# Kernel tuning notes

Hardware: AMD Instinct MI355X
Metric: run time of the kernel (lower is better)

The kernel has to match this reference:

```python
import jax, jax.numpy as jnp
import numpy as np

A, U, ANT, D2, H = 128, 8, 64, 64, 256
NUE = A * U            # 1024 ues
E_INT = A * NUE        # 131072 interferes edges (all ap x ue pairs)
E_DL = NUE             # one d_link edge per ue


def _mlp(x, Wa, ba, Wb, bb):
    return jax.nn.relu(x @ Wa + ba) @ Wb + bb


def setup_inputs() -> dict:
    key = jax.random.key(0)
    ks = jax.random.split(key, 14)
    f32 = jnp.float32
    inp = {
        'pl_int_re': jax.random.normal(ks[0], (E_INT, ANT), f32) * 0.1,
        'pl_int_im': jax.random.normal(ks[1], (E_INT, ANT), f32) * 0.1,
        'pl_dl_re': jax.random.normal(ks[2], (E_DL, ANT), f32) * 0.1,
        'pl_dl_im': jax.random.normal(ks[3], (E_DL, ANT), f32) * 0.1,
        'pv_re': jax.random.normal(ks[4], (A, U, ANT), f32) * 0.1,
        'pv_im': jax.random.normal(ks[5], (A, U, ANT), f32) * 0.1,
        'W2a': jax.random.normal(ks[6], (4 * ANT, H), f32) / np.sqrt(4 * ANT),
        'b2a': jnp.zeros((H,), f32),
        'W2b': jax.random.normal(ks[7], (H, D2), f32) / np.sqrt(H),
        'b2b': jnp.zeros((D2,), f32),
        'W1a': jax.random.normal(ks[8], (1 + 2 * ANT + D2, H), f32) / np.sqrt(1 + 2 * ANT + D2),
        'b1a': jnp.zeros((H,), f32),
        'W1b': jax.random.normal(ks[9], (H, 2 * ANT), f32) / np.sqrt(H),
        'b1b': jnp.zeros((2 * ANT,), f32),
        # interferes: every ap -> every ue
        'int_src': jnp.repeat(jnp.arange(A, dtype=jnp.int32), NUE),
        'int_dst': jnp.tile(jnp.arange(NUE, dtype=jnp.int32), A),
        # d_link: ap a -> ues [a*U, (a+1)*U)
        'dl_src': jnp.repeat(jnp.arange(A, dtype=jnp.int32), U),
        'dl_dst': jnp.arange(NUE, dtype=jnp.int32),
    }
    return inp


def reference(pl_int_re, pl_int_im, pl_dl_re, pl_dl_im, pv_re, pv_im,
              W2a, b2a, W2b, b2b, W1a, b1a, W1b, b1b,
              int_src, int_dst, dl_src, dl_dst):
    pv = jax.lax.complex(pv_re, pv_im)            # [A,U,ANT] ap power_vector
    pl_int = jax.lax.complex(pl_int_re, pl_int_im)  # [E_INT,ANT]
    pl_dl = jax.lax.complex(pl_dl_re, pl_dl_im)     # [E_DL,ANT]

    def aggregate_interferes(pv_cur):
        src_sum = jnp.sum(pv_cur, axis=1)[int_src]              # [E,ANT]
        infer_vec = src_sum.conj() * pl_int                      # [E,ANT]
        sum_ap = jnp.sum(jnp.abs(infer_vec) ** 2, axis=-1)       # ||.||^2 -> [E]
        return jax.ops.segment_sum(sum_ap[:, None], int_dst, num_segments=NUE)  # [NUE,1]

    # 1) aggregate_interferes (stored in graph; recomputed at the end)
    _ = aggregate_interferes(pv)

    # 2) mlp_aggregate_interferes
    src_sum = jnp.sum(pv, axis=1)[int_src]                       # [E,ANT] complex
    feats = jnp.concatenate([pl_int, src_sum], axis=1)           # [E,2*ANT] complex
    cat_feats = jnp.concatenate([feats.real, feats.imag], axis=1)  # [E,4*ANT]
    msg2 = _mlp(cat_feats, W2a, b2a, W2b, b2b)                   # [E,D2]
    mlp_ue_all = jax.ops.segment_sum(msg2, int_dst, num_segments=NUE)  # [NUE,D2]

    # 3) update_ue_power_vector (d_link edges)
    src_pv_dl = pv[dl_src]                                       # [E_DL,U,ANT]
    iner = jnp.einsum('eua,ea->eu', src_pv_dl.conj(), pl_dl)     # bmm -> [E_DL,U]
    norm1 = jnp.abs(iner) ** 2                                   # [E_DL,U]
    mask1 = jnp.ones((E_DL, U), norm1.dtype).at[jnp.arange(E_DL), dl_dst % U].set(0.0)
    in_infer = jnp.sum(norm1 * mask1, axis=1)[:, None]           # [E_DL,1]

    feat1 = jnp.concatenate([in_infer, pl_dl.real, pl_dl.imag, mlp_ue_all[dl_dst]], axis=1)
    out1 = _mlp(feat1, W1a, b1a, W1b, b1b).reshape(E_DL, 2, ANT)  # [E_DL,2,ANT]
    ue_pv_msg = jax.lax.complex(out1[:, 0, :], out1[:, 1, :])    # [E_DL,ANT]
    # each ue receives exactly one message
    ue_pv = jnp.zeros((NUE, ANT), ue_pv_msg.dtype).at[dl_dst].set(ue_pv_msg)

    # 4) update_ap_power_vector (u_link: ue i -> ap i//U; mailbox [A,U,ANT])
    mailbox = ue_pv.reshape(A, U, ANT)
    flat = mailbox.reshape(A, U * ANT)
    row_sums = jnp.sum(jnp.abs(flat), axis=-1, keepdims=True)
    pv_new = (flat / row_sums).reshape(A, U, ANT)

    # 5) final aggregate_interferes with updated power vectors
    ue_all_interference = aggregate_interferes(pv_new)

    out_stacked = jnp.stack([pv_new.real, pv_new.imag])          # [2,A,U,ANT]
    return out_stacked, ue_all_interference
```

## Files before the change

kernel.cpp:

```cpp
#include <hip/hip_runtime.h>
#include <hip/hip_bf16.h>
#include <hip/hip_fp16.h>

#define A_NUM 128
#define U_NUM 8
#define ANT 64
#define D2 64
#define H_DIM 256
#define NUE 1024
#define E_INT 131072

typedef __attribute__((ext_vector_type(8))) short bf16x8_t;
typedef __attribute__((ext_vector_type(4))) float f32x4_t;

static __device__ inline unsigned short f2bf(float x) {
    unsigned int u = __float_as_uint(x);
    unsigned int r = (u + 0x7fffu + ((u >> 16) & 1u)) >> 16;
    return (unsigned short)r;
}
static __device__ inline unsigned int pack2(float a, float b) {
    return (unsigned int)f2bf(a) | ((unsigned int)f2bf(b) << 16);
}
static __device__ inline float bf2f(unsigned short s) {
    return __uint_as_float(((unsigned int)s) << 16);
}

__global__ void prep_kernel(const float* __restrict__ pv_re, const float* __restrict__ pv_im,
                            const float* __restrict__ W2a, const float* __restrict__ b2a,
                            const float* __restrict__ W2b,
                            const float* __restrict__ W1a, const float* __restrict__ W1b,
                            float* __restrict__ Sa, unsigned short* __restrict__ WpT,
                            unsigned short* __restrict__ W2bT,
                            float* __restrict__ W1aT, float* __restrict__ W1bT) {
    int bid = blockIdx.x, t = threadIdx.x;
    if (bid < A_NUM) {
        __shared__ float sre[ANT], sim[ANT];
        if (t < ANT) {
            float s = 0.f;
            for (int u = 0; u < U_NUM; ++u) s += pv_re[bid * 512 + u * 64 + t];
            sre[t] = s;
        } else if (t < 2 * ANT) {
            int ant = t - ANT;
            float s = 0.f;
            for (int u = 0; u < U_NUM; ++u) s += pv_im[bid * 512 + u * 64 + ant];
            sim[ant] = s;
        }
        __syncthreads();
        float acc = b2a[t];
        for (int ant = 0; ant < ANT; ++ant) {
            acc += sre[ant] * W2a[(64 + ant) * H_DIM + t];
            acc += sim[ant] * W2a[(192 + ant) * H_DIM + t];
        }
        Sa[bid * H_DIM + t] = acc;
    } else if (bid < 136) {
        int base = (bid - A_NUM) * 256 + t;
        for (int i = base; i < 32768 + 16384; i += 8 * 256) {
            if (i < 32768) {
                int h = i >> 7, k = i & 127;
                int row = (k < 64) ? k : (k + 64);
                WpT[i] = f2bf(W2a[row * H_DIM + h]);
            } else {
                int i2 = i - 32768;
                int d = i2 >> 8, k2 = i2 & 255;
                W2bT[i2] = f2bf(W2b[k2 * D2 + d]);
            }
        }
    } else {
        for (int i = (bid - 136) * 256 + t; i < 53248 + 32768; i += 32 * 256) {
            if (i < 53248) {
                int h = i / 208, k = i % 208;
                W1aT[i] = (k < 193) ? W1a[k * 256 + h] : 0.f;
            } else {
                int i2 = i - 53248;
                int c = i2 >> 8, k = i2 & 255;
                W1bT[i2] = W1b[k * 128 + c];
            }
        }
    }
}

__global__ __launch_bounds__(256, 3) void mlp2_kernel(
        const float* __restrict__ plre, const float* __restrict__ plim,
        const float* __restrict__ Sa, const unsigned short* __restrict__ WpT,
        const unsigned short* __restrict__ W2bT, float* __restrict__ partial,
        unsigned short* __restrict__ Pws) {
    __shared__ __attribute__((aligned(16))) unsigned short F[32][136];
    __shared__ __attribute__((aligned(16))) unsigned short Hl[32][264];
    int bid = blockIdx.x;
    int jt_idx = bid & 31, ac = bid >> 5;
    int j0 = jt_idx * 32, a0 = ac * 8;
    int t = threadIdx.x, w = t >> 6, l = t & 63, lm = l & 15, lk = l >> 4;

    int er = t >> 3, seg = t & 7;
    const float* stage_base = (seg < 4) ? plre : plim;
    int stage_off = (j0 + er) * 64 + (seg & 3) * 16;
    int col = ((seg < 4) ? 0 : 64) + (seg & 3) * 16;

    f32x4_t acc2[2];
    acc2[0] = (f32x4_t){0.f, 0.f, 0.f, 0.f};
    acc2[1] = (f32x4_t){0.f, 0.f, 0.f, 0.f};

    float4 stg0, stg1, stg2, stg3;
    {
        const float* p = stage_base + a0 * 65536 + stage_off;
        stg0 = *reinterpret_cast<const float4*>(p);
        stg1 = *reinterpret_cast<const float4*>(p + 4);
        stg2 = *reinterpret_cast<const float4*>(p + 8);
        stg3 = *reinterpret_cast<const float4*>(p + 12);
    }

    for (int ai = 0; ai < 8; ++ai) {
        int a = a0 + ai;
        {
            unsigned int pk0 = pack2(stg0.x, stg0.y), pk1 = pack2(stg0.z, stg0.w);
            unsigned int pk2 = pack2(stg1.x, stg1.y), pk3 = pack2(stg1.z, stg1.w);
            unsigned int pk4 = pack2(stg2.x, stg2.y), pk5 = pack2(stg2.z, stg2.w);
            unsigned int pk6 = pack2(stg3.x, stg3.y), pk7 = pack2(stg3.z, stg3.w);
            *reinterpret_cast<uint4*>(&F[er][col]) = make_uint4(pk0, pk1, pk2, pk3);
            *reinterpret_cast<uint4*>(&F[er][col + 8]) = make_uint4(pk4, pk5, pk6, pk7);
        }
        __syncthreads();
        {
            uint4 rr = *reinterpret_cast<const uint4*>(&F[er][seg * 8]);
            uint4 ri = *reinterpret_cast<const uint4*>(&F[er][64 + seg * 8]);
            const unsigned short* pr = (const unsigned short*)&rr;
            const unsigned short* pi = (const unsigned short*)&ri;
            unsigned int pk[4];
#pragma unroll
            for (int i = 0; i < 4; ++i) {
                float re0 = bf2f(pr[2 * i]), im0 = bf2f(pi[2 * i]);
                float re1 = bf2f(pr[2 * i + 1]), im1 = bf2f(pi[2 * i + 1]);
                unsigned short h0 = __half_as_ushort(__float2half(re0 * re0 + im0 * im0));
                unsigned short h1 = __half_as_ushort(__float2half(re1 * re1 + im1 * im1));
                pk[i] = (unsigned int)h0 | ((unsigned int)h1 << 16);
            }
            *reinterpret_cast<uint4*>(&Pws[(unsigned)(a * 1024 + j0 + er) * 64 + seg * 8]) =
                make_uint4(pk[0], pk[1], pk[2], pk[3]);
        }
        if (ai < 7) {
            const float* p = stage_base + (a0 + ai + 1) * 65536 + stage_off;
            stg0 = *reinterpret_cast<const float4*>(p);
            stg1 = *reinterpret_cast<const float4*>(p + 4);
            stg2 = *reinterpret_cast<const float4*>(p + 8);
            stg3 = *reinterpret_cast<const float4*>(p + 12);
        }
        f32x4_t acc1[2][4];
#pragma unroll
        for (int ht = 0; ht < 4; ++ht) {
            float sa = Sa[a * H_DIM + w * 64 + ht * 16 + lm];
            f32x4_t v = (f32x4_t){sa, sa, sa, sa};
            acc1[0][ht] = v;
            acc1[1][ht] = v;
        }
#pragma unroll
        for (int kc = 0; kc < 4; ++kc) {
            bf16x8_t bfr[4];
#pragma unroll
            for (int ht = 0; ht < 4; ++ht) {
                int h = w * 64 + ht * 16 + lm;
                bfr[ht] = *reinterpret_cast<const bf16x8_t*>(WpT + h * 128 + kc * 32 + lk * 8);
            }
#pragma unroll
            for (int jt = 0; jt < 2; ++jt) {
                bf16x8_t afr = *reinterpret_cast<const bf16x8_t*>(&F[jt * 16 + lm][kc * 32 + lk * 8]);
#pragma unroll
                for (int ht = 0; ht < 4; ++ht)
                    acc1[jt][ht] = __builtin_amdgcn_mfma_f32_16x16x32_bf16(afr, bfr[ht], acc1[jt][ht], 0, 0, 0);
            }
        }
#pragma unroll
        for (int jt = 0; jt < 2; ++jt)
#pragma unroll
            for (int ht = 0; ht < 4; ++ht)
#pragma unroll
                for (int r = 0; r < 4; ++r) {
                    int j = jt * 16 + lk * 4 + r;
                    int h = w * 64 + ht * 16 + lm;
                    float v = acc1[jt][ht][r];
                    Hl[j][h] = f2bf(v > 0.f ? v : 0.f);
                }
        __syncthreads();
        int d = w * 16 + lm;
#pragma unroll
        for (int kc = 0; kc < 8; ++kc) {
            bf16x8_t b2 = *reinterpret_cast<const bf16x8_t*>(W2bT + d * 256 + kc * 32 + lk * 8);
#pragma unroll
            for (int jt = 0; jt < 2; ++jt) {
                bf16x8_t a2 = *reinterpret_cast<const bf16x8_t*>(&Hl[jt * 16 + lm][kc * 32 + lk * 8]);
                acc2[jt] = __builtin_amdgcn_mfma_f32_16x16x32_bf16(a2, b2, acc2[jt], 0, 0, 0);
            }
        }
    }
#pragma unroll
    for (int jt = 0; jt < 2; ++jt)
#pragma unroll
        for (int r = 0; r < 4; ++r) {
            int j = j0 + jt * 16 + lk * 4 + r;
            int d = w * 16 + lm;
            partial[ac * 65536 + j * 64 + d] = acc2[jt][r];
        }
}

__global__ __launch_bounds__(512) void dlink_norm(
        const float* __restrict__ pv_re, const float* __restrict__ pv_im,
        const float* __restrict__ pldre, const float* __restrict__ pldim,
        const float* __restrict__ partial, const float* __restrict__ b2b,
        const float* __restrict__ W1aT, const float* __restrict__ b1a,
        const float* __restrict__ W1bT, const float* __restrict__ b1b,
        float* __restrict__ Q, float* __restrict__ out) {
    int a = blockIdx.x, t = threadIdx.x, w = t >> 6, l = t & 63;
    __shared__ float pvr[512], pvi[512], pldr[512], pldi[512];
    __shared__ float nrm[8][8];
    __shared__ __attribute__((aligned(16))) float feat[8][212];
    __shared__ __attribute__((aligned(16))) float h1[8][260];
    __shared__ float red2[2][8][128];
    __shared__ __attribute__((aligned(16))) float o1[8][128];
    __shared__ float redn[8];
    __shared__ float SshInv;

    pvr[t] = pv_re[a * 512 + t];
    pvi[t] = pv_im[a * 512 + t];
    pldr[t] = pldre[a * 512 + t];
    pldi[t] = pldim[a * 512 + t];
    {
        float acc = 128.f * b2b[t & 63];
#pragma unroll
        for (int c = 0; c < 16; ++c) acc += partial[c * 65536 + a * 512 + t];
        feat[t >> 6][129 + (t & 63)] = acc;
    }
    if (t < 152) feat[t / 19][193 + t % 19] = 0.f;
    __syncthreads();
    feat[t >> 6][1 + (t & 63)] = pldr[t];
    feat[t >> 6][65 + (t & 63)] = pldi[t];
#pragma unroll
    for (int p = 0; p < 8; ++p) {
        int idx = w * 8 + p;
        int el = idx >> 3, u = idx & 7;
        float pr = pvr[u * 64 + l], pi = pvi[u * 64 + l];
        float qr = pldr[el * 64 + l], qi = pldi[el * 64 + l];
        float ir = pr * qr + pi * qi;
        float ii = pr * qi - pi * qr;
        for (int m = 1; m < 64; m <<= 1) {
            ir += __shfl_xor(ir, m, 64);
            ii += __shfl_xor(ii, m, 64);
        }
        if (l == 0) nrm[el][u] = ir * ir + ii * ii;
    }
    __syncthreads();
    if (t < 8) {
        float s = 0.f;
        for (int u = 0; u < 8; ++u)
            if (u != t) s += nrm[t][u];
        feat[t][0] = s;
    }
    __syncthreads();
    {
        int h = t >> 1, e0 = (t & 1) * 4;
        const float4* wrow = reinterpret_cast<const float4*>(W1aT + h * 208);
        const float4* f0p = reinterpret_cast<const float4*>(&feat[e0 + 0][0]);
        const float4* f1p = reinterpret_cast<const float4*>(&feat[e0 + 1][0]);
        const float4* f2p = reinterpret_cast<const float4*>(&feat[e0 + 2][0]);
        const float4* f3p = reinterpret_cast<const float4*>(&feat[e0 + 3][0]);
        float ac0 = 0.f, ac1 = 0.f, ac2 = 0.f, ac3 = 0.f;
#pragma unroll 4
        for (int kq = 0; kq < 52; ++kq) {
            float4 wv = wrow[kq];
            float4 f0 = f0p[kq], f1 = f1p[kq], f2 = f2p[kq], f3 = f3p[kq];
            ac0 = fmaf(wv.x, f0.x, ac0); ac0 = fmaf(wv.y, f0.y, ac0);
            ac0 = fmaf(wv.z, f0.z, ac0); ac0 = fmaf(wv.w, f0.w, ac0);
            ac1 = fmaf(wv.x, f1.x, ac1); ac1 = fmaf(wv.y, f1.y, ac1);
            ac1 = fmaf(wv.z, f1.z, ac1); ac1 = fmaf(wv.w, f1.w, ac1);
            ac2 = fmaf(wv.x, f2.x, ac2); ac2 = fmaf(wv.y, f2.y, ac2);
            ac2 = fmaf(wv.z, f2.z, ac2); ac2 = fmaf(wv.w, f2.w, ac2);
            ac3 = fmaf(wv.x, f3.x, ac3); ac3 = fmaf(wv.y, f3.y, ac3);
            ac3 = fmaf(wv.z, f3.z, ac3); ac3 = fmaf(wv.w, f3.w, ac3);
        }
        float bb = b1a[h];
        float s0 = bb + ac0, s1 = bb + ac1, s2 = bb + ac2, s3 = bb + ac3;
        h1[e0 + 0][h] = s0 > 0.f ? s0 : 0.f;
        h1[e0 + 1][h] = s1 > 0.f ? s1 : 0.f;
        h1[e0 + 2][h] = s2 > 0.f ? s2 : 0.f;
        h1[e0 + 3][h] = s3 > 0.f ? s3 : 0.f;
    }
    __syncthreads();
    {
        int e0 = (t & 1) * 4, c = (t >> 1) & 127, kh = t >> 8;
        const float4* wrow = reinterpret_cast<const float4*>(W1bT + c * 256 + kh * 128);
        const float4* g0 = reinterpret_cast<const float4*>(&h1[e0 + 0][kh * 128]);
        const float4* g1 = reinterpret_cast<const float4*>(&h1[e0 + 1][kh * 128]);
        const float4* g2 = reinterpret_cast<const float4*>(&h1[e0 + 2][kh * 128]);
        const float4* g3 = reinterpret_cast<const float4*>(&h1[e0 + 3][kh * 128]);
        float ac0 = 0.f, ac1 = 0.f, ac2 = 0.f, ac3 = 0.f;
#pragma unroll 4
        for (int kq = 0; kq < 32; ++kq) {
            float4 wv = wrow[kq];
            float4 f0 = g0[kq], f1 = g1[kq], f2 = g2[kq], f3 = g3[kq];
            ac0 = fmaf(wv.x, f0.x, ac0); ac0 = fmaf(wv.y, f0.y, ac0);
            ac0 = fmaf(wv.z, f0.z, ac0); ac0 = fmaf(wv.w, f0.w, ac0);
            ac1 = fmaf(wv.x, f1.x, ac1); ac1 = fmaf(wv.y, f1.y, ac1);
            ac1 = fmaf(wv.z, f1.z, ac1); ac1 = fmaf(wv.w, f1.w, ac1);
            ac2 = fmaf(wv.x, f2.x, ac2); ac2 = fmaf(wv.y, f2.y, ac2);
            ac2 = fmaf(wv.z, f2.z, ac2); ac2 = fmaf(wv.w, f2.w, ac2);
            ac3 = fmaf(wv.x, f3.x, ac3); ac3 = fmaf(wv.y, f3.y, ac3);
            ac3 = fmaf(wv.z, f3.z, ac3); ac3 = fmaf(wv.w, f3.w, ac3);
        }
        red2[kh][e0 + 0][c] = ac0;
        red2[kh][e0 + 1][c] = ac1;
        red2[kh][e0 + 2][c] = ac2;
        red2[kh][e0 + 3][c] = ac3;
    }
    __syncthreads();
    {
        int i0 = t, i1 = t + 512;
        o1[i0 >> 7][i0 & 127] = b1b[i0 & 127] + red2[0][i0 >> 7][i0 & 127] + red2[1][i0 >> 7][i0 & 127];
        o1[i1 >> 7][i1 & 127] = b1b[i1 & 127] + red2[0][i1 >> 7][i1 & 127] + red2[1][i1 >> 7][i1 & 127];
    }
    __syncthreads();
    {
        int el = t >> 6, ant = t & 63;
        float re = o1[el][ant], im = o1[el][64 + ant];
        float v = sqrtf(re * re + im * im);
        for (int m = 1; m < 64; m <<= 1) v += __shfl_xor(v, m, 64);
        if (l == 0) redn[w] = v;
    }
    __syncthreads();
    if (t == 0) {
        float S = redn[0] + redn[1] + redn[2] + redn[3] +
                  redn[4] + redn[5] + redn[6] + redn[7];
        SshInv = 1.f / S;
    }
    __syncthreads();
    {
        float inv = SshInv;
        int el = t >> 6, ant = t & 63;
        out[a * 512 + t] = o1[el][ant] * inv;
        out[65536 + a * 512 + t] = o1[el][64 + ant] * inv;
        if (t < 64) {
            float sr = 0.f, si = 0.f;
#pragma unroll
            for (int u = 0; u < 8; ++u) {
                sr += o1[u][t];
                si += o1[u][64 + t];
            }
            sr *= inv;
            si *= inv;
            Q[a * 64 + t] = sr * sr + si * si;
        }
    }
}

__global__ __launch_bounds__(256) void final_agg(const unsigned short* __restrict__ Pws,
                                                 const float* __restrict__ Qv,
                                                 float* __restrict__ out) {
    int bid = blockIdx.x, t = threadIdx.x, w = t >> 6, l = t & 63;
    __shared__ __attribute__((aligned(16))) float Qc[128][68];
    for (int i = t; i < 8192; i += 256) Qc[i >> 6][i & 63] = Qv[i];
    __syncthreads();
    int j = bid * 4 + w;
    int as = l >> 3, og = l & 7;
    float acc = 0.f;
#pragma unroll 4
    for (int ab = 0; ab < 16; ++ab) {
        int aa = ab * 8 + as;
        uint4 pv4 = *reinterpret_cast<const uint4*>(&Pws[(unsigned)(aa * 1024 + j) * 64 + og * 8]);
        float4 q0 = *reinterpret_cast<const float4*>(&Qc[aa][og * 8]);
        float4 q1 = *reinterpret_cast<const float4*>(&Qc[aa][og * 8 + 4]);
        const unsigned short* hp = (const unsigned short*)&pv4;
        acc += __half2float(__ushort_as_half(hp[0])) * q0.x;
        acc += __half2float(__ushort_as_half(hp[1])) * q0.y;
        acc += __half2float(__ushort_as_half(hp[2])) * q0.z;
        acc += __half2float(__ushort_as_half(hp[3])) * q0.w;
        acc += __half2float(__ushort_as_half(hp[4])) * q1.x;
        acc += __half2float(__ushort_as_half(hp[5])) * q1.y;
        acc += __half2float(__ushort_as_half(hp[6])) * q1.z;
        acc += __half2float(__ushort_as_half(hp[7])) * q1.w;
    }
    for (int m = 1; m < 64; m <<= 1) acc += __shfl_xor(acc, m, 64);
    if (l == 0) out[131072 + j] = acc;
}

extern "C" void kernel_launch(void* const* d_in, const int* in_sizes, int n_in,
                              void* d_out, int out_size, void* d_ws, size_t ws_size,
                              hipStream_t stream) {
    const float* plre = (const float*)d_in[0];
    const float* plim = (const float*)d_in[1];
    const float* pldre = (const float*)d_in[2];
    const float* pldim = (const float*)d_in[3];
    const float* pvre = (const float*)d_in[4];
    const float* pvim = (const float*)d_in[5];
    const float* W2a = (const float*)d_in[6];
    const float* b2a = (const float*)d_in[7];
    const float* W2b = (const float*)d_in[8];
    const float* b2b = (const float*)d_in[9];
    const float* W1a = (const float*)d_in[10];
    const float* b1a = (const float*)d_in[11];
    const float* W1b = (const float*)d_in[12];
    const float* b1b = (const float*)d_in[13];

    char* ws = (char*)d_ws;
    float* Sa = (float*)(ws);
    unsigned short* WpT = (unsigned short*)(ws + 131072);
    unsigned short* W2bT = (unsigned short*)(ws + 196608);
    float* Q = (float*)(ws + 229376);
    float* partial = (float*)(ws + 262144);
    unsigned short* Pws = (unsigned short*)(ws + 4456448);
    float* W1aT = (float*)(ws + 21233664);
    float* W1bT = (float*)(ws + 21446656);
    float* out = (float*)d_out;

    prep_kernel<<<168, 256, 0, stream>>>(pvre, pvim, W2a, b2a, W2b, W1a, W1b,
                                         Sa, WpT, W2bT, W1aT, W1bT);
    mlp2_kernel<<<512, 256, 0, stream>>>(plre, plim, Sa, WpT, W2bT, partial, Pws);
    dlink_norm<<<128, 512, 0, stream>>>(pvre, pvim, pldre, pldim, partial, b2b,
                                        W1aT, b1a, W1bT, b1b, Q, out);
    final_agg<<<256, 256, 0, stream>>>(Pws, Q, out);
}
```

Before: 76.87 us.

## Restructure mlp2 kernel: register-resident weights, double-buffered LDS, per-wave K-split

The mlp2 kernel now loads its W2a and W2b weight fragments into registers once per block instead of re-reading them every iteration. It double-buffers the feature tile in LDS with an XOR swizzle, so only one barrier is needed per iteration and the next tile's global loads overlap the current tile's compute. The second GEMM is split across waves along K, and each wave keeps its hidden tile in a private LDS slice. A final LDS reduction then writes vectorized partial results. The prep kernel's Sa dot product also gets multiple accumulators. The cost is higher register pressure (occupancy bound lowered from 3 to 2 blocks) and extra LDS for the reduction buffer.

```diff
diff --git a/kernel.cpp b/kernel.cpp
--- a/kernel.cpp
+++ b/kernel.cpp
@@ -46,12 +46,14 @@
             sim[ant] = s;
         }
         __syncthreads();
-        float acc = b2a[t];
-        for (int ant = 0; ant < ANT; ++ant) {
-            acc += sre[ant] * W2a[(64 + ant) * H_DIM + t];
-            acc += sim[ant] * W2a[(192 + ant) * H_DIM + t];
-        }
-        Sa[bid * H_DIM + t] = acc;
+        float a0 = 0.f, a1 = 0.f, a2 = 0.f, a3 = 0.f;
+        for (int ant = 0; ant < ANT; ant += 2) {
+            a0 += sre[ant] * W2a[(64 + ant) * H_DIM + t];
+            a1 += sim[ant] * W2a[(192 + ant) * H_DIM + t];
+            a2 += sre[ant + 1] * W2a[(64 + ant + 1) * H_DIM + t];
+            a3 += sim[ant + 1] * W2a[(192 + ant + 1) * H_DIM + t];
+        }
+        Sa[bid * H_DIM + t] = b2a[t] + ((a0 + a2) + (a1 + a3));
     } else if (bid < 136) {
         int base = (bid - A_NUM) * 256 + t;
         for (int i = base; i < 32768 + 16384; i += 8 * 256) {
@@ -79,50 +81,78 @@
     }
 }
 
-__global__ __launch_bounds__(256, 3) void mlp2_kernel(
+__global__ __launch_bounds__(256, 2) void mlp2_kernel(
         const float* __restrict__ plre, const float* __restrict__ plim,
         const float* __restrict__ Sa, const unsigned short* __restrict__ WpT,
         const unsigned short* __restrict__ W2bT, float* __restrict__ partial,
         unsigned short* __restrict__ Pws) {
-    __shared__ __attribute__((aligned(16))) unsigned short F[32][136];
-    __shared__ __attribute__((aligned(16))) unsigned short Hl[32][264];
+    __shared__ __attribute__((aligned(16))) unsigned short F2[2][4096];
+    __shared__ __attribute__((aligned(16))) unsigned short Hl[4][2048];
+    __shared__ __attribute__((aligned(16))) float red[4][32][68];
     int bid = blockIdx.x;
     int jt_idx = bid & 31, ac = bid >> 5;
     int j0 = jt_idx * 32, a0 = ac * 8;
     int t = threadIdx.x, w = t >> 6, l = t & 63, lm = l & 15, lk = l >> 4;
 
+    bf16x8_t bfr[4][4];
+#pragma unroll
+    for (int ht = 0; ht < 4; ++ht)
+#pragma unroll
+        for (int kc = 0; kc < 4; ++kc)
+            bfr[ht][kc] = *reinterpret_cast<const bf16x8_t*>(
+                WpT + (w * 64 + ht * 16 + lm) * 128 + kc * 32 + lk * 8);
+    bf16x8_t b2h[4][2];
+#pragma unroll
+    for (int dt = 0; dt < 4; ++dt)
+#pragma unroll
+        for (int kcl = 0; kcl < 2; ++kcl)
+            b2h[dt][kcl] = *reinterpret_cast<const bf16x8_t*>(
+                W2bT + (dt * 16 + lm) * 256 + w * 64 + kcl * 32 + lk * 8);
+
     int er = t >> 3, seg = t & 7;
     const float* stage_base = (seg < 4) ? plre : plim;
     int stage_off = (j0 + er) * 64 + (seg & 3) * 16;
-    int col = ((seg < 4) ? 0 : 64) + (seg & 3) * 16;
-
-    f32x4_t acc2[2];
-    acc2[0] = (f32x4_t){0.f, 0.f, 0.f, 0.f};
-    acc2[1] = (f32x4_t){0.f, 0.f, 0.f, 0.f};
-
-    float4 stg0, stg1, stg2, stg3;
+    int colu = ((seg < 4) ? 0 : 64) + (seg & 3) * 16;
+    int widx0 = (er * 128 + colu) ^ ((er & 7) << 3);
+    int widx1 = (er * 128 + colu + 8) ^ ((er & 7) << 3);
+
+    f32x4_t acc2[4][2];
+#pragma unroll
+    for (int dt = 0; dt < 4; ++dt)
+#pragma unroll
+        for (int jt = 0; jt < 2; ++jt)
+            acc2[dt][jt] = (f32x4_t){0.f, 0.f, 0.f, 0.f};
+
+    float4 s0, s1, s2, s3;
     {
         const float* p = stage_base + a0 * 65536 + stage_off;
-        stg0 = *reinterpret_cast<const float4*>(p);
-        stg1 = *reinterpret_cast<const float4*>(p + 4);
-        stg2 = *reinterpret_cast<const float4*>(p + 8);
-        stg3 = *reinterpret_cast<const float4*>(p + 12);
-    }
-
+        s0 = *reinterpret_cast<const float4*>(p);
+        s1 = *reinterpret_cast<const float4*>(p + 4);
+        s2 = *reinterpret_cast<const float4*>(p + 8);
+        s3 = *reinterpret_cast<const float4*>(p + 12);
+        unsigned int pk0 = pack2(s0.x, s0.y), pk1 = pack2(s0.z, s0.w);
+        unsigned int pk2 = pack2(s1.x, s1.y), pk3 = pack2(s1.z, s1.w);
+        unsigned int pk4 = pack2(s2.x, s2.y), pk5 = pack2(s2.z, s2.w);
+        unsigned int pk6 = pack2(s3.x, s3.y), pk7 = pack2(s3.z, s3.w);
+        *reinterpret_cast<uint4*>(&F2[0][widx0]) = make_uint4(pk0, pk1, pk2, pk3);
+        *reinterpret_cast<uint4*>(&F2[0][widx1]) = make_uint4(pk4, pk5, pk6, pk7);
+    }
+    {
+        const float* p = stage_base + (a0 + 1) * 65536 + stage_off;
+        s0 = *reinterpret_cast<const float4*>(p);
+        s1 = *reinterpret_cast<const float4*>(p + 4);
+        s2 = *reinterpret_cast<const float4*>(p + 8);
+        s3 = *reinterpret_cast<const float4*>(p + 12);
+    }
+    __syncthreads();
+
+    int cur = 0;
     for (int ai = 0; ai < 8; ++ai) {
         int a = a0 + ai;
+        const unsigned short* Fc = F2[cur];
         {
-            unsigned int pk0 = pack2(stg0.x, stg0.y), pk1 = pack2(stg0.z, stg0.w);
-            unsigned int pk2 = pack2(stg1.x, stg1.y), pk3 = pack2(stg1.z, stg1.w);
-            unsigned int pk4 = pack2(stg2.x, stg2.y), pk5 = pack2(stg2.z, stg2.w);
-            unsigned int pk6 = pack2(stg3.x, stg3.y), pk7 = pack2(stg3.z, stg3.w);
-            *reinterpret_cast<uint4*>(&F[er][col]) = make_uint4(pk0, pk1, pk2, pk3);
-            *reinterpret_cast<uint4*>(&F[er][col + 8]) = make_uint4(pk4, pk5, pk6, pk7);
-        }
-        __syncthreads();
-        {
-            uint4 rr = *reinterpret_cast<const uint4*>(&F[er][seg * 8]);
-            uint4 ri = *reinterpret_cast<const uint4*>(&F[er][64 + seg * 8]);
+            uint4 rr = *reinterpret_cast<const uint4*>(Fc + ((er * 128 + seg * 8) ^ ((er & 7) << 3)));
+            uint4 ri = *reinterpret_cast<const uint4*>(Fc + ((er * 128 + 64 + seg * 8) ^ ((er & 7) << 3)));
             const unsigned short* pr = (const unsigned short*)&rr;
             const unsigned short* pi = (const unsigned short*)&ri;
             unsigned int pk[4];
@@ -137,37 +167,25 @@
             *reinterpret_cast<uint4*>(&Pws[(unsigned)(a * 1024 + j0 + er) * 64 + seg * 8]) =
                 make_uint4(pk[0], pk[1], pk[2], pk[3]);
         }
-        if (ai < 7) {
-            const float* p = stage_base + (a0 + ai + 1) * 65536 + stage_off;
-            stg0 = *reinterpret_cast<const float4*>(p);
-            stg1 = *reinterpret_cast<const float4*>(p + 4);
-            stg2 = *reinterpret_cast<const float4*>(p + 8);
-            stg3 = *reinterpret_cast<const float4*>(p + 12);
-        }
+        float sa[4];
+#pragma unroll
+        for (int ht = 0; ht < 4; ++ht) sa[ht] = Sa[a * H_DIM + w * 64 + ht * 16 + lm];
         f32x4_t acc1[2][4];
 #pragma unroll
-        for (int ht = 0; ht < 4; ++ht) {
-            float sa = Sa[a * H_DIM + w * 64 + ht * 16 + lm];
-            f32x4_t v = (f32x4_t){sa, sa, sa, sa};
-            acc1[0][ht] = v;
-            acc1[1][ht] = v;
-        }
-#pragma unroll
-        for (int kc = 0; kc < 4; ++kc) {
-            bf16x8_t bfr[4];
-#pragma unroll
-            for (int ht = 0; ht < 4; ++ht) {
-                int h = w * 64 + ht * 16 + lm;
-                bfr[ht] = *reinterpret_cast<const bf16x8_t*>(WpT + h * 128 + kc * 32 + lk * 8);
-            }
+        for (int jt = 0; jt < 2; ++jt)
+#pragma unroll
+            for (int ht = 0; ht < 4; ++ht)
+                acc1[jt][ht] = (f32x4_t){sa[ht], sa[ht], sa[ht], sa[ht]};
+#pragma unroll
+        for (int kc = 0; kc < 4; ++kc)
 #pragma unroll
             for (int jt = 0; jt < 2; ++jt) {
-                bf16x8_t afr = *reinterpret_cast<const bf16x8_t*>(&F[jt * 16 + lm][kc * 32 + lk * 8]);
+                bf16x8_t afr = *reinterpret_cast<const bf16x8_t*>(
+                    Fc + (((jt * 16 + lm) * 128 + kc * 32 + lk * 8) ^ ((lm & 7) << 3)));
 #pragma unroll
                 for (int ht = 0; ht < 4; ++ht)
-                    acc1[jt][ht] = __builtin_amdgcn_mfma_f32_16x16x32_bf16(afr, bfr[ht], acc1[jt][ht], 0, 0, 0);
-            }
-        }
+                    acc1[jt][ht] = __builtin_amdgcn_mfma_f32_16x16x32_bf16(afr, bfr[ht][kc], acc1[jt][ht], 0, 0, 0);
+            }
 #pragma unroll
         for (int jt = 0; jt < 2; ++jt)
 #pragma unroll
@@ -175,30 +193,56 @@
 #pragma unroll
                 for (int r = 0; r < 4; ++r) {
                     int j = jt * 16 + lk * 4 + r;
-                    int h = w * 64 + ht * 16 + lm;
                     float v = acc1[jt][ht][r];
-                    Hl[j][h] = f2bf(v > 0.f ? v : 0.f);
+                    Hl[w][((j << 6) + ht * 16 + lm) ^ ((j & 7) << 3)] = f2bf(v > 0.f ? v : 0.f);
                 }
-        __syncthreads();
-        int d = w * 16 + lm;
-#pragma unroll
-        for (int kc = 0; kc < 8; ++kc) {
-            bf16x8_t b2 = *reinterpret_cast<const bf16x8_t*>(W2bT + d * 256 + kc * 32 + lk * 8);
+#pragma unroll
+        for (int kcl = 0; kcl < 2; ++kcl)
 #pragma unroll
             for (int jt = 0; jt < 2; ++jt) {
-                bf16x8_t a2 = *reinterpret_cast<const bf16x8_t*>(&Hl[jt * 16 + lm][kc * 32 + lk * 8]);
-                acc2[jt] = __builtin_amdgcn_mfma_f32_16x16x32_bf16(a2, b2, acc2[jt], 0, 0, 0);
-            }
-        }
-    }
-#pragma unroll
-    for (int jt = 0; jt < 2; ++jt)
-#pragma unroll
-        for (int r = 0; r < 4; ++r) {
-            int j = j0 + jt * 16 + lk * 4 + r;
-            int d = w * 16 + lm;
-            partial[ac * 65536 + j * 64 + d] = acc2[jt][r];
-        }
+                bf16x8_t a2 = *reinterpret_cast<const bf16x8_t*>(
+                    &Hl[w][(((jt * 16 + lm) << 6) + kcl * 32 + lk * 8) ^ ((lm & 7) << 3)]);
+#pragma unroll
+                for (int dt = 0; dt < 4; ++dt)
+                    acc2[dt][jt] = __builtin_amdgcn_mfma_f32_16x16x32_bf16(a2, b2h[dt][kcl], acc2[dt][jt], 0, 0, 0);
+            }
+        if (ai < 7) {
+            unsigned int pk0 = pack2(s0.x, s0.y), pk1 = pack2(s0.z, s0.w);
+            unsigned int pk2 = pack2(s1.x, s1.y), pk3 = pack2(s1.z, s1.w);
+            unsigned int pk4 = pack2(s2.x, s2.y), pk5 = pack2(s2.z, s2.w);
+            unsigned int pk6 = pack2(s3.x, s3.y), pk7 = pack2(s3.z, s3.w);
+            *reinterpret_cast<uint4*>(&F2[cur ^ 1][widx0]) = make_uint4(pk0, pk1, pk2, pk3);
+            *reinterpret_cast<uint4*>(&F2[cur ^ 1][widx1]) = make_uint4(pk4, pk5, pk6, pk7);
+            if (ai < 6) {
+                const float* p = stage_base + (a0 + ai + 2) * 65536 + stage_off;
+                s0 = *reinterpret_cast<const float4*>(p);
+                s1 = *reinterpret_cast<const float4*>(p + 4);
+                s2 = *reinterpret_cast<const float4*>(p + 8);
+                s3 = *reinterpret_cast<const float4*>(p + 12);
+            }
+            __syncthreads();
+            cur ^= 1;
+        }
+    }
+#pragma unroll
+    for (int dt = 0; dt < 4; ++dt)
+#pragma unroll
+        for (int jt = 0; jt < 2; ++jt)
+#pragma unroll
+            for (int r = 0; r < 4; ++r)
+                red[w][jt * 16 + lk * 4 + r][dt * 16 + lm] = acc2[dt][jt][r];
+    __syncthreads();
+    {
+        int j = t >> 3, d0 = (t & 7) * 8;
+        float s[8];
+#pragma unroll
+        for (int i = 0; i < 8; ++i)
+            s[i] = (red[0][j][d0 + i] + red[1][j][d0 + i]) +
+                   (red[2][j][d0 + i] + red[3][j][d0 + i]);
+        float* dst = partial + ac * 65536 + (j0 + j) * 64 + d0;
+        *reinterpret_cast<float4*>(dst) = make_float4(s[0], s[1], s[2], s[3]);
+        *reinterpret_cast<float4*>(dst + 4) = make_float4(s[4], s[5], s[6], s[7]);
+    }
 }
 
 __global__ __launch_bounds__(512) void dlink_norm(
```

Result: faster. 66.70 us (-13.2%).

## Restructure mlp2 with 16-row tiles, register-resident weights and double-buffered staging

Applied to the files above, without the earlier changes.

The mlp2 kernel now tiles 16 UE rows per block instead of 32, doubling the grid to 1024 blocks. It keeps the W2a-slice and W2b bf16 fragments in registers for the whole block rather than reloading them every AP iteration. The input staging is double-buffered in LDS so the next AP's path-loss tile is packed while the current one is computed, and launch bounds are raised to 4 blocks per SIMD. The prep kernel also switches to coalesced reads for the W1a/W1b transposes and splits the Sa dot product across several accumulators; the register-held weights risk register pressure under the tighter launch bound.

```diff
diff --git a/kernel.cpp b/kernel.cpp
--- a/kernel.cpp
+++ b/kernel.cpp
@@ -46,12 +46,14 @@
             sim[ant] = s;
         }
         __syncthreads();
-        float acc = b2a[t];
-        for (int ant = 0; ant < ANT; ++ant) {
-            acc += sre[ant] * W2a[(64 + ant) * H_DIM + t];
-            acc += sim[ant] * W2a[(192 + ant) * H_DIM + t];
-        }
-        Sa[bid * H_DIM + t] = acc;
+        float a0 = 0.f, a1 = 0.f, a2 = 0.f, a3 = 0.f;
+        for (int ant = 0; ant < ANT; ant += 2) {
+            a0 += sre[ant] * W2a[(64 + ant) * H_DIM + t];
+            a1 += sim[ant] * W2a[(192 + ant) * H_DIM + t];
+            a2 += sre[ant + 1] * W2a[(64 + ant + 1) * H_DIM + t];
+            a3 += sim[ant + 1] * W2a[(192 + ant + 1) * H_DIM + t];
+        }
+        Sa[bid * H_DIM + t] = b2a[t] + ((a0 + a2) + (a1 + a3));
     } else if (bid < 136) {
         int base = (bid - A_NUM) * 256 + t;
         for (int i = base; i < 32768 + 16384; i += 8 * 256) {
@@ -68,61 +70,73 @@
     } else {
         for (int i = (bid - 136) * 256 + t; i < 53248 + 32768; i += 32 * 256) {
             if (i < 53248) {
-                int h = i / 208, k = i % 208;
-                W1aT[i] = (k < 193) ? W1a[k * 256 + h] : 0.f;
+                int k = i >> 8, h = i & 255;
+                W1aT[h * 208 + k] = (k < 193) ? W1a[k * 256 + h] : 0.f;
             } else {
                 int i2 = i - 53248;
-                int c = i2 >> 8, k = i2 & 255;
-                W1bT[i2] = W1b[k * 128 + c];
-            }
-        }
-    }
-}
-
-__global__ __launch_bounds__(256, 3) void mlp2_kernel(
+                int k = i2 >> 7, c = i2 & 127;
+                W1bT[c * 256 + k] = W1b[k * 128 + c];
+            }
+        }
+    }
+}
+
+__global__ __launch_bounds__(256, 4) void mlp2_kernel(
         const float* __restrict__ plre, const float* __restrict__ plim,
         const float* __restrict__ Sa, const unsigned short* __restrict__ WpT,
         const unsigned short* __restrict__ W2bT, float* __restrict__ partial,
         unsigned short* __restrict__ Pws) {
-    __shared__ __attribute__((aligned(16))) unsigned short F[32][136];
-    __shared__ __attribute__((aligned(16))) unsigned short Hl[32][264];
+    __shared__ __attribute__((aligned(16))) unsigned short F2[2][16 * 136];
+    __shared__ __attribute__((aligned(16))) unsigned short Hl[16][264];
     int bid = blockIdx.x;
-    int jt_idx = bid & 31, ac = bid >> 5;
-    int j0 = jt_idx * 32, a0 = ac * 8;
+    int ac = bid >> 6, jt = bid & 63;
+    int j0 = jt * 16, a0 = ac * 8;
     int t = threadIdx.x, w = t >> 6, l = t & 63, lm = l & 15, lk = l >> 4;
 
-    int er = t >> 3, seg = t & 7;
-    const float* stage_base = (seg < 4) ? plre : plim;
-    int stage_off = (j0 + er) * 64 + (seg & 3) * 16;
-    int col = ((seg < 4) ? 0 : 64) + (seg & 3) * 16;
-
-    f32x4_t acc2[2];
-    acc2[0] = (f32x4_t){0.f, 0.f, 0.f, 0.f};
-    acc2[1] = (f32x4_t){0.f, 0.f, 0.f, 0.f};
-
-    float4 stg0, stg1, stg2, stg3;
-    {
-        const float* p = stage_base + a0 * 65536 + stage_off;
-        stg0 = *reinterpret_cast<const float4*>(p);
-        stg1 = *reinterpret_cast<const float4*>(p + 4);
-        stg2 = *reinterpret_cast<const float4*>(p + 8);
-        stg3 = *reinterpret_cast<const float4*>(p + 12);
-    }
-
+    bf16x8_t bfr[4][4];
+#pragma unroll
+    for (int ht = 0; ht < 4; ++ht)
+#pragma unroll
+        for (int kc = 0; kc < 4; ++kc)
+            bfr[ht][kc] = *reinterpret_cast<const bf16x8_t*>(
+                WpT + (w * 64 + ht * 16 + lm) * 128 + kc * 32 + lk * 8);
+    bf16x8_t b2h[8];
+#pragma unroll
+    for (int kcl = 0; kcl < 8; ++kcl)
+        b2h[kcl] = *reinterpret_cast<const bf16x8_t*>(
+            W2bT + (w * 16 + lm) * 256 + kcl * 32 + lk * 8);
+
+    int er = t >> 4, seg = t & 15;
+    const float* stage_base = (seg < 8) ? plre : plim;
+    int stage_off = (j0 + er) * 64 + (seg & 7) * 8;
+    int fw = er * 136 + seg * 8;
+
+    f32x4_t acc2 = (f32x4_t){0.f, 0.f, 0.f, 0.f};
+
+    float4 s0, s1;
+    {
+        const float* p = stage_base + (size_t)a0 * 65536 + stage_off;
+        s0 = *reinterpret_cast<const float4*>(p);
+        s1 = *reinterpret_cast<const float4*>(p + 4);
+        *reinterpret_cast<uint4*>(&F2[0][fw]) =
+            make_uint4(pack2(s0.x, s0.y), pack2(s0.z, s0.w),
+                       pack2(s1.x, s1.y), pack2(s1.z, s1.w));
+    }
+    {
+        const float* p = stage_base + (size_t)(a0 + 1) * 65536 + stage_off;
+        s0 = *reinterpret_cast<const float4*>(p);
+        s1 = *reinterpret_cast<const float4*>(p + 4);
+    }
+
+    int cur = 0;
     for (int ai = 0; ai < 8; ++ai) {
         int a = a0 + ai;
-        {
-            unsigned int pk0 = pack2(stg0.x, stg0.y), pk1 = pack2(stg0.z, stg0.w);
-            unsigned int pk2 = pack2(stg1.x, stg1.y), pk3 = pack2(stg1.z, stg1.w);
-            unsigned int pk4 = pack2(stg2.x, stg2.y), pk5 = pack2(stg2.z, stg2.w);
-            unsigned int pk6 = pack2(stg3.x, stg3.y), pk7 = pack2(stg3.z, stg3.w);
-            *reinterpret_cast<uint4*>(&F[er][col]) = make_uint4(pk0, pk1, pk2, pk3);
-            *reinterpret_cast<uint4*>(&F[er][col + 8]) = make_uint4(pk4, pk5, pk6, pk7);
-        }
         __syncthreads();
-        {
-            uint4 rr = *reinterpret_cast<const uint4*>(&F[er][seg * 8]);
-            uint4 ri = *reinterpret_cast<const uint4*>(&F[er][64 + seg * 8]);
+        const unsigned short* Fc = F2[cur];
+        if (t < 128) {
+            int er3 = t >> 3, seg3 = t & 7;
+            uint4 rr = *reinterpret_cast<const uint4*>(Fc + er3 * 136 + seg3 * 8);
+            uint4 ri = *reinterpret_cast<const uint4*>(Fc + er3 * 136 + 64 + seg3 * 8);
             const unsigned short* pr = (const unsigned short*)&rr;
             const unsigned short* pi = (const unsigned short*)&ri;
             unsigned int pk[4];
@@ -134,71 +148,50 @@
                 unsigned short h1 = __half_as_ushort(__float2half(re1 * re1 + im1 * im1));
                 pk[i] = (unsigned int)h0 | ((unsigned int)h1 << 16);
             }
-            *reinterpret_cast<uint4*>(&Pws[(unsigned)(a * 1024 + j0 + er) * 64 + seg * 8]) =
+            *reinterpret_cast<uint4*>(&Pws[(unsigned)(a * 1024 + j0 + er3) * 64 + seg3 * 8]) =
                 make_uint4(pk[0], pk[1], pk[2], pk[3]);
         }
-        if (ai < 7) {
-            const float* p = stage_base + (a0 + ai + 1) * 65536 + stage_off;
-            stg0 = *reinterpret_cast<const float4*>(p);
-            stg1 = *reinterpret_cast<const float4*>(p + 4);
-            stg2 = *reinterpret_cast<const float4*>(p + 8);
-            stg3 = *reinterpret_cast<const float4*>(p + 12);
-        }
-        f32x4_t acc1[2][4];
+        f32x4_t acc1[4];
 #pragma unroll
         for (int ht = 0; ht < 4; ++ht) {
             float sa = Sa[a * H_DIM + w * 64 + ht * 16 + lm];
-            f32x4_t v = (f32x4_t){sa, sa, sa, sa};
-            acc1[0][ht] = v;
-            acc1[1][ht] = v;
+            acc1[ht] = (f32x4_t){sa, sa, sa, sa};
         }
 #pragma unroll
         for (int kc = 0; kc < 4; ++kc) {
-            bf16x8_t bfr[4];
-#pragma unroll
-            for (int ht = 0; ht < 4; ++ht) {
-                int h = w * 64 + ht * 16 + lm;
-                bfr[ht] = *reinterpret_cast<const bf16x8_t*>(WpT + h * 128 + kc * 32 + lk * 8);
-            }
-#pragma unroll
-            for (int jt = 0; jt < 2; ++jt) {
-                bf16x8_t afr = *reinterpret_cast<const bf16x8_t*>(&F[jt * 16 + lm][kc * 32 + lk * 8]);
-#pragma unroll
-                for (int ht = 0; ht < 4; ++ht)
-                    acc1[jt][ht] = __builtin_amdgcn_mfma_f32_16x16x32_bf16(afr, bfr[ht], acc1[jt][ht], 0, 0, 0);
-            }
-        }
-#pragma unroll
-        for (int jt = 0; jt < 2; ++jt)
+            bf16x8_t afr = *reinterpret_cast<const bf16x8_t*>(Fc + lm * 136 + kc * 32 + lk * 8);
 #pragma unroll
             for (int ht = 0; ht < 4; ++ht)
-#pragma unroll
-                for (int r = 0; r < 4; ++r) {
-                    int j = jt * 16 + lk * 4 + r;
-                    int h = w * 64 + ht * 16 + lm;
-                    float v = acc1[jt][ht][r];
-                    Hl[j][h] = f2bf(v > 0.f ? v : 0.f);
-                }
+                acc1[ht] = __builtin_amdgcn_mfma_f32_16x16x32_bf16(afr, bfr[ht][kc], acc1[ht], 0, 0, 0);
+        }
+#pragma unroll
+        for (int ht = 0; ht < 4; ++ht)
+#pragma unroll
+            for (int r = 0; r < 4; ++r) {
+                float v = acc1[ht][r];
+                Hl[lk * 4 + r][ht * 16 + lm + w * 64] = f2bf(v > 0.f ? v : 0.f);
+            }
         __syncthreads();
-        int d = w * 16 + lm;
-#pragma unroll
-        for (int kc = 0; kc < 8; ++kc) {
-            bf16x8_t b2 = *reinterpret_cast<const bf16x8_t*>(W2bT + d * 256 + kc * 32 + lk * 8);
-#pragma unroll
-            for (int jt = 0; jt < 2; ++jt) {
-                bf16x8_t a2 = *reinterpret_cast<const bf16x8_t*>(&Hl[jt * 16 + lm][kc * 32 + lk * 8]);
-                acc2[jt] = __builtin_amdgcn_mfma_f32_16x16x32_bf16(a2, b2, acc2[jt], 0, 0, 0);
-            }
-        }
-    }
-#pragma unroll
-    for (int jt = 0; jt < 2; ++jt)
-#pragma unroll
-        for (int r = 0; r < 4; ++r) {
-            int j = j0 + jt * 16 + lk * 4 + r;
-            int d = w * 16 + lm;
-            partial[ac * 65536 + j * 64 + d] = acc2[jt][r];
-        }
+#pragma unroll
+        for (int kcl = 0; kcl < 8; ++kcl) {
+            bf16x8_t a2 = *reinterpret_cast<const bf16x8_t*>(&Hl[lm][kcl * 32 + lk * 8]);
+            acc2 = __builtin_amdgcn_mfma_f32_16x16x32_bf16(a2, b2h[kcl], acc2, 0, 0, 0);
+        }
+        if (ai < 7) {
+            *reinterpret_cast<uint4*>(&F2[cur ^ 1][fw]) =
+                make_uint4(pack2(s0.x, s0.y), pack2(s0.z, s0.w),
+                           pack2(s1.x, s1.y), pack2(s1.z, s1.w));
+            if (ai < 6) {
+                const float* p = stage_base + (size_t)(a0 + ai + 2) * 65536 + stage_off;
+                s0 = *reinterpret_cast<const float4*>(p);
+                s1 = *reinterpret_cast<const float4*>(p + 4);
+            }
+            cur ^= 1;
+        }
+    }
+#pragma unroll
+    for (int r = 0; r < 4; ++r)
+        partial[ac * 65536 + (j0 + lk * 4 + r) * 64 + w * 16 + lm] = acc2[r];
 }
 
 __global__ __launch_bounds__(512) void dlink_norm(
@@ -410,7 +403,7 @@
 
     prep_kernel<<<168, 256, 0, stream>>>(pvre, pvim, W2a, b2a, W2b, W1a, W1b,
                                          Sa, WpT, W2bT, W1aT, W1bT);
-    mlp2_kernel<<<512, 256, 0, stream>>>(plre, plim, Sa, WpT, W2bT, partial, Pws);
+    mlp2_kernel<<<1024, 256, 0, stream>>>(plre, plim, Sa, WpT, W2bT, partial, Pws);
     dlink_norm<<<128, 512, 0, stream>>>(pvre, pvim, pldre, pldim, partial, b2b,
                                         W1aT, b1a, W1bT, b1b, Q, out);
     final_agg<<<256, 256, 0, stream>>>(Pws, Q, out);
```

After: 78.70 us. +2.4%, slower.
